# Performance work log

Measured on AMD Instinct MI355X. Metric: run time of the kernel, lower is better.

## Reference

```python
import jax, jax.numpy as jnp
import numpy as np

B, S, H, NH, HD = 2, 2048, 1024, 16, 64
THETA = 10000.0


def setup_inputs() -> dict:
    key = jax.random.key(0)
    k1, k2, k3, k4, k5 = jax.random.split(key, 5)
    hidden_states = jax.random.normal(k1, (B, S, H), dtype=jnp.float32)
    # RoPE tables, interleaved-pair layout: [c0,c0,c1,c1,...] along head_dim
    inv_freq = 1.0 / (THETA ** (jnp.arange(0, HD, 2, dtype=jnp.float32) / HD))
    t = jnp.arange(S, dtype=jnp.float32)
    freqs = jnp.outer(t, inv_freq)                      # [S, HD//2]
    freqs_cos = jnp.repeat(jnp.cos(freqs), 2, axis=-1)  # [S, HD]
    freqs_sin = jnp.repeat(jnp.sin(freqs), 2, axis=-1)  # [S, HD]
    position_ids = jnp.arange(S, dtype=jnp.int32)
    w = 0.02
    Wq = jax.random.normal(k2, (H, H), dtype=jnp.float32) * w
    Wk = jax.random.normal(k3, (H, H), dtype=jnp.float32) * w
    Wv = jax.random.normal(k4, (H, H), dtype=jnp.float32) * w
    Wo = jax.random.normal(k5, (H, H), dtype=jnp.float32) * w
    return {"hidden_states": hidden_states, "freqs_cos": freqs_cos,
            "freqs_sin": freqs_sin, "position_ids": position_ids,
            "Wq": Wq, "Wk": Wk, "Wv": Wv, "Wo": Wo}


def _rotate_half_interleaved(x):
    # stack([-x[..., 1::2], x[..., ::2]], -1).reshape_as(x)
    xe = x.reshape(x.shape[:-1] + (HD // 2, 2))
    return jnp.stack([-xe[..., 1], xe[..., 0]], axis=-1).reshape(x.shape)


def reference(hidden_states, freqs_cos, freqs_sin, position_ids, Wq, Wk, Wv, Wo):
    b, s, _ = hidden_states.shape
    # QKV projections (torch Linear: y = x @ W.T), split into heads [b, nh, s, hd]
    q = jnp.einsum('bsh,oh->bso', hidden_states, Wq).reshape(b, s, NH, HD).transpose(0, 2, 1, 3)
    k = jnp.einsum('bsh,oh->bso', hidden_states, Wk).reshape(b, s, NH, HD).transpose(0, 2, 1, 3)
    v = jnp.einsum('bsh,oh->bso', hidden_states, Wv).reshape(b, s, NH, HD).transpose(0, 2, 1, 3)
    cos = freqs_cos[position_ids][None, None]  # [1, 1, s, hd]
    sin = freqs_sin[position_ids][None, None]
    rq = _rotate_half_interleaved(q)
    # NOTE: faithful to source bug — rotate_half_k is built from q, not k
    q = q * cos + rq * sin
    k = k * cos + rq * sin
    # causal SDPA, scale = 1/sqrt(head_dim)
    scores = jnp.einsum('bhqd,bhkd->bhqk', q, k) / jnp.sqrt(jnp.float32(HD))
    causal = jnp.tril(jnp.ones((s, s), dtype=bool))
    scores = jnp.where(causal, scores, jnp.float32(-1e30))
    attn = jax.nn.softmax(scores, axis=-1)
    out = jnp.einsum('bhqk,bhkd->bhqd', attn, v)
    out = out.transpose(0, 2, 1, 3).reshape(b, s, H)
    return jnp.einsum('bsh,oh->bso', out, Wo)
```

## Files before the change

### kernel.cpp

```cpp
#include <hip/hip_runtime.h>
#include <stdint.h>

#define BB 2
#define SS 2048
#define HH 1024
#define NHH 16
#define HDD 64

typedef short bf16s;
typedef __attribute__((ext_vector_type(8))) short short8;
typedef __attribute__((ext_vector_type(4))) short short4v;
typedef __attribute__((ext_vector_type(2))) short short2v;
typedef __attribute__((ext_vector_type(4))) float f32x4;
typedef _Float16 half4v __attribute__((ext_vector_type(4)));
typedef _Float16 half8v __attribute__((ext_vector_type(8)));
typedef __fp16 fp16x2 __attribute__((ext_vector_type(2)));

__device__ inline short f2bf(float f) {
  union { float f; uint32_t u; } v; v.f = f;
  uint32_t r = (v.u + 0x7fffu + ((v.u >> 16) & 1u)) >> 16;
  return (short)r;
}
__device__ inline float bf2f(short h) {
  union { uint32_t u; float f; } v; v.u = ((uint32_t)(uint16_t)h) << 16;
  return v.f;
}

__device__ __forceinline__ float exp2_raw(float x) {
  float r;
  asm("v_exp_f32 %0, %1\n\ts_nop 0" : "=v"(r) : "v"(x));
  return r;
}

__device__ inline void gld_lds16(const void* g, void* l) {
  __builtin_amdgcn_global_load_lds((const __attribute__((address_space(1))) void*)g,
                                   (__attribute__((address_space(3))) void*)l, 16, 0, 0);
}

__device__ inline void stv(short* C, size_t i, float v) { C[i] = f2bf(v); }
__device__ inline void stv(float* C, size_t i, float v) { C[i] = v; }

__device__ inline f32x4 mfma_k32(short8 a, short8 b, f32x4 c) {
  return __builtin_amdgcn_mfma_f32_16x16x32_bf16(a, b, c, 0, 0, 0);
}
__device__ inline f32x4 mfma_k32(half8v a, half8v b, f32x4 c) {
  return __builtin_amdgcn_mfma_f32_16x16x32_f16(a, b, c, 0, 0, 0);
}
template <typename ET> struct ftr;
template <> struct ftr<short>     { using v8 = short8; };
template <> struct ftr<_Float16>  { using v8 = half8v; };

__global__ __launch_bounds__(256) void convert_all(
    const float* __restrict__ x, const float* __restrict__ Wq,
    const float* __restrict__ Wk, const float* __restrict__ Wv,
    const float* __restrict__ Wo, bf16s* __restrict__ xb,
    bf16s* __restrict__ wqkv, _Float16* __restrict__ wof) {
  const long M1 = 1024L * 1024L;
  long e = (long)(blockIdx.x * blockDim.x + threadIdx.x) * 4;
  if (e < 7 * M1) {
    const float* src; bf16s* dst;
    if (e < 4 * M1)      { src = x  + e;            dst = xb   + e; }
    else if (e < 5 * M1) { src = Wq + (e - 4 * M1); dst = wqkv + (e - 4 * M1); }
    else if (e < 6 * M1) { src = Wk + (e - 5 * M1); dst = wqkv + (e - 4 * M1); }
    else                 { src = Wv + (e - 6 * M1); dst = wqkv + (e - 4 * M1); }
    float4 v = *(const float4*)src;
    short4v o;
    o.x = f2bf(v.x); o.y = f2bf(v.y); o.z = f2bf(v.z); o.w = f2bf(v.w);
    *(short4v*)dst = o;
  } else {
    float4 v = *(const float4*)(Wo + (e - 7 * M1));
    half4v o;
    o.x = (_Float16)v.x; o.y = (_Float16)v.y;
    o.z = (_Float16)v.z; o.w = (_Float16)v.w;
    *(half4v*)(wof + (e - 7 * M1)) = o;
  }
}

template <typename ET, typename OT, int MT>
__global__ __launch_bounds__(256) void gemm_bt(
    const ET* __restrict__ A, const ET* __restrict__ Bm,
    OT* __restrict__ C, int K, int ldc) {
  using V8 = typename ftr<ET>::v8;
  __shared__ __align__(16) ET As[MT * 32 * 64];
  __shared__ __align__(16) ET Bs[128 * 64];
  const int tid = threadIdx.x;
  const int lane = tid & 63, w = tid >> 6;
  const int quad = lane >> 4, mcol = lane & 15;
  const int bm = blockIdx.y * (MT * 32), bn = blockIdx.x * 128;
  const int wm = (w >> 1) * (MT * 16), wn = (w & 1) * 64;
  f32x4 acc[MT][4] = {};
  const int nkt = K >> 6;
  for (int kt = 0; kt < nkt; ++kt) {
    __syncthreads();
#pragma unroll
    for (int i = 0; i < MT; ++i) {
      int seg = (i * 4 + w) * 512;
      int flat = seg + lane * 8;
      int row = flat >> 6;
      int cpos = (flat >> 3) & 7;
      int cs = cpos ^ (row & 7);
      gld_lds16(A + (size_t)(bm + row) * K + kt * 64 + cs * 8, &As[seg]);
    }
#pragma unroll
    for (int i = 0; i < 4; ++i) {
      int seg = (i * 4 + w) * 512;
      int flat = seg + lane * 8;
      int row = flat >> 6;
      int cpos = (flat >> 3) & 7;
      int cs = cpos ^ (row & 7);
      gld_lds16(Bm + (size_t)(bn + row) * K + kt * 64 + cs * 8, &Bs[seg]);
    }
    __syncthreads();
#pragma unroll
    for (int ks = 0; ks < 2; ++ks) {
      V8 af[MT], bf[4];
#pragma unroll
      for (int mt = 0; mt < MT; ++mt) {
        int row = wm + mt * 16 + mcol;
        int cs = (ks * 4 + quad) ^ (row & 7);
        af[mt] = *(const V8*)&As[row * 64 + cs * 8];
      }
#pragma unroll
      for (int nt = 0; nt < 4; ++nt) {
        int row = wn + nt * 16 + mcol;
        int cs = (ks * 4 + quad) ^ (row & 7);
        bf[nt] = *(const V8*)&Bs[row * 64 + cs * 8];
      }
#pragma unroll
      for (int mt = 0; mt < MT; ++mt)
#pragma unroll
        for (int nt = 0; nt < 4; ++nt)
          acc[mt][nt] = mfma_k32(af[mt], bf[nt], acc[mt][nt]);
    }
  }
#pragma unroll
  for (int mt = 0; mt < MT; ++mt)
#pragma unroll
    for (int nt = 0; nt < 4; ++nt) {
      int r0 = bm + wm + mt * 16 + quad * 4;
      int c = bn + wn + nt * 16 + mcol;
#pragma unroll
      for (int r = 0; r < 4; ++r)
        stv(C, (size_t)(r0 + r) * ldc + c, acc[mt][nt][r]);
    }
}

__global__ __launch_bounds__(256) void postproc(
    const bf16s* __restrict__ qkv, const float* __restrict__ fcos,
    const float* __restrict__ fsin, const int* __restrict__ pos,
    bf16s* __restrict__ Q, bf16s* __restrict__ Kc, _Float16* __restrict__ Vt) {
  const float LOG2E = 1.4426950408889634f;
  const int st = blockIdx.x, bh = blockIdx.y;
  const int b = bh >> 4, h = bh & 15;
  const int tid = threadIdx.x;
  const int m0 = b * 2048 + st * 64;
  {
    const int row = tid >> 2, pc = tid & 3;
    const int s = st * 64 + row;
    const int p = pos[s];
    const bf16s* qp = qkv + (size_t)(m0 + row) * 3072 + h * 64 + pc * 16;
    short8 qv[2] = { *(const short8*)qp, *(const short8*)(qp + 8) };
    short8 kv[2] = { *(const short8*)(qp + 1024), *(const short8*)(qp + 1032) };
    const float* cp = fcos + (size_t)p * 64 + pc * 16;
    const float* sp = fsin + (size_t)p * 64 + pc * 16;
    short8 qo[2], ko[2];
#pragma unroll
    for (int hf = 0; hf < 2; ++hf)
#pragma unroll
      for (int j = 0; j < 4; ++j) {
        float c = cp[hf * 8 + 2 * j], sn = sp[hf * 8 + 2 * j];
        float q0 = bf2f(qv[hf][2 * j]), q1 = bf2f(qv[hf][2 * j + 1]);
        float k0 = bf2f(kv[hf][2 * j]), k1 = bf2f(kv[hf][2 * j + 1]);
        qo[hf][2 * j]     = f2bf((q0 * c - q1 * sn) * 0.125f);
        qo[hf][2 * j + 1] = f2bf((q1 * c + q0 * sn) * 0.125f);
        ko[hf][2 * j]     = f2bf((k0 * c - q1 * sn) * LOG2E);
        ko[hf][2 * j + 1] = f2bf((k1 * c + q0 * sn) * LOG2E);
      }
    size_t o = ((size_t)bh * 2048 + s) * 64 + pc * 16;
    *(short8*)&Q[o] = qo[0];  *(short8*)&Q[o + 8] = qo[1];
    *(short8*)&Kc[o] = ko[0]; *(short8*)&Kc[o + 8] = ko[1];
  }
  __shared__ __align__(16) _Float16 T[64 * 72];
#pragma unroll
  for (int p2 = 0; p2 < 2; ++p2) {
    int sl = p2 * 32 + (tid >> 3);
    int ch = tid & 7;
    short8 v = *(const short8*)&qkv[(size_t)(m0 + sl) * 3072 + 2048 + h * 64 + ch * 8];
#pragma unroll
    for (int j = 0; j < 8; ++j) T[(ch * 8 + j) * 72 + sl] = (_Float16)bf2f(v[j]);
  }
  __syncthreads();
#pragma unroll
  for (int p2 = 0; p2 < 2; ++p2) {
    int dl = p2 * 32 + (tid >> 3);
    int ch = tid & 7;
    half8v v = *(const half8v*)&T[dl * 72 + ch * 8];
    *(half8v*)&Vt[((size_t)bh * 64 + dl) * 2048 + st * 64 + ch * 8] = v;
  }
}

template <bool DOB>
__device__ __forceinline__ void step2(
    const bf16s* __restrict__ Ks, const _Float16* __restrict__ Vp,
    const short8* bqA, const short8* bqB,
    f32x4* OA, f32x4* OB, float& lA, float& lB,
    bool diagA, bool diagB, int w, int quad, int col) {
  f32x4 sA[4], sB[4];
#pragma unroll
  for (int t = 0; t < 4; ++t) {
    f32x4 a = {}, bb = {};
#pragma unroll
    for (int ks = 0; ks < 2; ++ks) {
      int krow = t * 16 + col;
      int cs = (ks * 4 + quad) ^ (krow & 7);
      short8 af = *(const short8*)&Ks[krow * 64 + cs * 8];
      a = __builtin_amdgcn_mfma_f32_16x16x32_bf16(af, bqA[ks], a, 0, 0, 0);
      if (DOB) bb = __builtin_amdgcn_mfma_f32_16x16x32_bf16(af, bqB[ks], bb, 0, 0, 0);
    }
    sA[t] = a;
    if (DOB) sB[t] = bb;
  }
  if (diagA) {
#pragma unroll
    for (int t = 0; t < 4; ++t)
#pragma unroll
      for (int r = 0; r < 4; ++r)
        if (t * 16 + quad * 4 + r > w * 16 + col) sA[t][r] = -1e30f;
  }
  if (DOB && diagB) {
#pragma unroll
    for (int t = 0; t < 4; ++t)
#pragma unroll
      for (int r = 0; r < 4; ++r)
        if (t * 16 + quad * 4 + r > w * 16 + col) sB[t][r] = -1e30f;
  }
  half4v paA[4], paB[4];
#pragma unroll
  for (int t = 0; t < 4; ++t) {
    {
      float p0 = exp2_raw(sA[t][0]), p1 = exp2_raw(sA[t][1]);
      float p2 = exp2_raw(sA[t][2]), p3 = exp2_raw(sA[t][3]);
      lA += (p0 + p1) + (p2 + p3);
      union { fp16x2 h2[2]; half4v h4; } u;
      u.h2[0] = __builtin_amdgcn_cvt_pkrtz(p0, p1);
      u.h2[1] = __builtin_amdgcn_cvt_pkrtz(p2, p3);
      paA[t] = u.h4;
    }
    if (DOB) {
      float p0 = exp2_raw(sB[t][0]), p1 = exp2_raw(sB[t][1]);
      float p2 = exp2_raw(sB[t][2]), p3 = exp2_raw(sB[t][3]);
      lB += (p0 + p1) + (p2 + p3);
      union { fp16x2 h2[2]; half4v h4; } u;
      u.h2[0] = __builtin_amdgcn_cvt_pkrtz(p0, p1);
      u.h2[1] = __builtin_amdgcn_cvt_pkrtz(p2, p3);
      paB[t] = u.h4;
    }
  }
#pragma unroll
  for (int dt = 0; dt < 4; ++dt) {
    int vrow = dt * 16 + col;
    const _Float16* vp = &Vp[vrow * 72 + (quad ^ (vrow & 3)) * 16];
    union { half8v v8; half4v v4[2]; } a01, a23;
    a01.v8 = *(const half8v*)vp;
    a23.v8 = *(const half8v*)(vp + 8);
    half4v bv[4] = { a01.v4[0], a01.v4[1], a23.v4[0], a23.v4[1] };
#pragma unroll
    for (int t = 0; t < 4; ++t) {
      OA[dt] = __builtin_amdgcn_mfma_f32_16x16x16f16(paA[t], bv[t], OA[dt], 0, 0, 0);
      if (DOB) OB[dt] = __builtin_amdgcn_mfma_f32_16x16x16f16(paB[t], bv[t], OB[dt], 0, 0, 0);
    }
  }
}

__global__ __launch_bounds__(256) void attn(
    const bf16s* __restrict__ Q, const bf16s* __restrict__ Kb,
    const _Float16* __restrict__ Vt, _Float16* __restrict__ O) {
  __shared__ __align__(16) bf16s Ks[64 * 64];
  __shared__ __align__(16) _Float16 Vp[64 * 72];
  const int bh = blockIdx.y;
  const int tid = threadIdx.x, lane = tid & 63, w = tid >> 6;
  const int quad = lane >> 4, col = lane & 15;
  const size_t base = (size_t)bh * 2048 * 64;
  const _Float16* vbase = Vt + (size_t)bh * 64 * 2048;
  const int b = bh >> 4, h = bh & 15;
  const int x = blockIdx.x;
  const int qbA = 31 - x, qbB = x;

  short8 bqA[2], bqB[2];
  {
    const int qrA = qbA * 64 + w * 16 + col;
    const int qrB = qbB * 64 + w * 16 + col;
#pragma unroll
    for (int ks = 0; ks < 2; ++ks) {
      bqA[ks] = *(const short8*)&Q[base + (size_t)qrA * 64 + ks * 32 + quad * 8];
      bqB[ks] = *(const short8*)&Q[base + (size_t)qrB * 64 + ks * 32 + quad * 8];
    }
  }
  f32x4 OA[4] = {}, OB[4] = {};
  float lA = 0.f, lB = 0.f;

  const int vd = tid >> 2, vc = tid & 3;
  const int rot = vd & 3;
  for (int kt = 0; kt <= qbA; ++kt) {
    half8v vr0 = *(const half8v*)&vbase[(size_t)vd * 2048 + kt * 64 + vc * 16];
    half8v vr1 = *(const half8v*)&vbase[(size_t)vd * 2048 + kt * 64 + vc * 16 + 8];
    __syncthreads();
    {
      union { half8v v8; half4v v4[2]; } u0, u1;
      u0.v8 = vr0; u1.v8 = vr1;
      int rbase = vd * 72 + vc * 4;
      *(half4v*)&Vp[rbase + (0 ^ rot) * 16] = u0.v4[0];
      *(half4v*)&Vp[rbase + (1 ^ rot) * 16] = u0.v4[1];
      *(half4v*)&Vp[rbase + (2 ^ rot) * 16] = u1.v4[0];
      *(half4v*)&Vp[rbase + (3 ^ rot) * 16] = u1.v4[1];
    }
#pragma unroll
    for (int i = 0; i < 2; ++i) {
      int seg = (i * 4 + w) * 512;
      int flat = seg + lane * 8;
      int row = flat >> 6, cpos = (flat >> 3) & 7;
      int cs = cpos ^ (row & 7);
      gld_lds16(&Kb[base + (size_t)(kt * 64 + row) * 64 + cs * 8], &Ks[seg]);
    }
    __syncthreads();
    if (kt <= qbB)
      step2<true>(Ks, Vp, bqA, bqB, OA, OB, lA, lB,
                  false, kt == qbB, w, quad, col);
    else
      step2<false>(Ks, Vp, bqA, bqB, OA, OB, lA, lB,
                   kt == qbA, false, w, quad, col);
  }

  lA += __shfl_xor(lA, 16); lA += __shfl_xor(lA, 32);
  lB += __shfl_xor(lB, 16); lB += __shfl_xor(lB, 32);

#pragma unroll
  for (int which = 0; which < 2; ++which) {
    const int qb = which ? qbB : qbA;
    const f32x4* Oacc = which ? OB : OA;
    const float l = which ? lB : lA;
    float l4[4];
#pragma unroll
    for (int r = 0; r < 4; ++r) l4[r] = __shfl(l, quad * 4 + r);
#pragma unroll
    for (int dt = 0; dt < 4; ++dt)
#pragma unroll
      for (int r = 0; r < 4; ++r) {
        int srow = qb * 64 + w * 16 + quad * 4 + r;
        O[((size_t)b * 2048 + srow) * 1024 + h * 64 + dt * 16 + col] =
            (_Float16)(Oacc[dt][r] / l4[r]);
      }
  }
}

extern "C" void kernel_launch(void* const* d_in, const int* in_sizes, int n_in,
                              void* d_out, int out_size, void* d_ws, size_t ws_size,
                              hipStream_t stream) {
  (void)in_sizes; (void)n_in; (void)out_size; (void)ws_size;
  const float* x  = (const float*)d_in[0];
  const float* fc = (const float*)d_in[1];
  const float* fs = (const float*)d_in[2];
  const int* pos  = (const int*)d_in[3];
  const float* Wq = (const float*)d_in[4];
  const float* Wk = (const float*)d_in[5];
  const float* Wv = (const float*)d_in[6];
  const float* Wo = (const float*)d_in[7];
  float* out = (float*)d_out;
  char* ws = (char*)d_ws;
  const size_t MB = 1024 * 1024;
  bf16s* xb    = (bf16s*)(ws);
  bf16s* wqkv  = (bf16s*)(ws + 8 * MB);
  _Float16* wof = (_Float16*)(ws + 14 * MB);
  bf16s* qkv   = (bf16s*)(ws + 16 * MB);
  bf16s* Qb    = (bf16s*)(ws + 40 * MB);
  bf16s* Kb    = (bf16s*)(ws + 48 * MB);
  _Float16* Vt = (_Float16*)(ws + 56 * MB);
  _Float16* Ob = (_Float16*)(ws);

  convert_all<<<8192, 256, 0, stream>>>(x, Wq, Wk, Wv, Wo, xb, wqkv, wof);
  gemm_bt<short, short, 4><<<dim3(24, 32), 256, 0, stream>>>(xb, wqkv, qkv, 1024, 3072);
  postproc<<<dim3(32, 32), 256, 0, stream>>>(qkv, fc, fs, pos, Qb, Kb, Vt);
  attn<<<dim3(16, 32), 256, 0, stream>>>(Qb, Kb, Vt, Ob);
  gemm_bt<_Float16, float, 2><<<dim3(8, 64), 256, 0, stream>>>(Ob, wof, out, 1024, 1024);
}
```

Baseline: 191.3 us.

## Split paired query-block attention into one query block per workgroup

The attention kernel no longer pairs a short and a long causal query block in each workgroup. It now launches 32x32 workgroups that each handle a single query block, processed in reverse order so the heaviest blocks start first. The V tile layout in LDS also changes from a rotated 72-stride layout to a plain 68-stride layout with half4 loads. This drops the K-fragment sharing between the two query blocks and the workgroup-level load balancing, and relies on more workgroups and hardware scheduling to balance the causal work instead. The new LDS stride may also cause bank conflicts on the V reads.

Result: slower. 209.0 us (+9.3%).

```diff
diff --git a/kernel.cpp b/kernel.cpp
--- a/kernel.cpp
+++ b/kernel.cpp
@@ -199,121 +199,81 @@
   }
 }
 
-template <bool DOB>
-__device__ __forceinline__ void step2(
-    const bf16s* __restrict__ Ks, const _Float16* __restrict__ Vp,
-    const short8* bqA, const short8* bqB,
-    f32x4* OA, f32x4* OB, float& lA, float& lB,
-    bool diagA, bool diagB, int w, int quad, int col) {
-  f32x4 sA[4], sB[4];
+__device__ __forceinline__ void attn_step(
+    const bf16s* __restrict__ Ks, const _Float16* __restrict__ Vs,
+    const short8* bq, f32x4* Oacc, float& l, bool diag,
+    int w, int quad, int col) {
+  f32x4 sc[4];
 #pragma unroll
   for (int t = 0; t < 4; ++t) {
-    f32x4 a = {}, bb = {};
+    f32x4 s4 = {};
 #pragma unroll
     for (int ks = 0; ks < 2; ++ks) {
       int krow = t * 16 + col;
       int cs = (ks * 4 + quad) ^ (krow & 7);
       short8 af = *(const short8*)&Ks[krow * 64 + cs * 8];
-      a = __builtin_amdgcn_mfma_f32_16x16x32_bf16(af, bqA[ks], a, 0, 0, 0);
-      if (DOB) bb = __builtin_amdgcn_mfma_f32_16x16x32_bf16(af, bqB[ks], bb, 0, 0, 0);
-    }
-    sA[t] = a;
-    if (DOB) sB[t] = bb;
-  }
-  if (diagA) {
+      s4 = __builtin_amdgcn_mfma_f32_16x16x32_bf16(af, bq[ks], s4, 0, 0, 0);
+    }
+    sc[t] = s4;
+  }
+  if (diag) {
 #pragma unroll
     for (int t = 0; t < 4; ++t)
 #pragma unroll
       for (int r = 0; r < 4; ++r)
-        if (t * 16 + quad * 4 + r > w * 16 + col) sA[t][r] = -1e30f;
-  }
-  if (DOB && diagB) {
-#pragma unroll
-    for (int t = 0; t < 4; ++t)
-#pragma unroll
-      for (int r = 0; r < 4; ++r)
-        if (t * 16 + quad * 4 + r > w * 16 + col) sB[t][r] = -1e30f;
-  }
-  half4v paA[4], paB[4];
+        if (t * 16 + quad * 4 + r > w * 16 + col) sc[t][r] = -1e30f;
+  }
+  half4v pa[4];
 #pragma unroll
   for (int t = 0; t < 4; ++t) {
-    {
-      float p0 = exp2_raw(sA[t][0]), p1 = exp2_raw(sA[t][1]);
-      float p2 = exp2_raw(sA[t][2]), p3 = exp2_raw(sA[t][3]);
-      lA += (p0 + p1) + (p2 + p3);
-      union { fp16x2 h2[2]; half4v h4; } u;
-      u.h2[0] = __builtin_amdgcn_cvt_pkrtz(p0, p1);
-      u.h2[1] = __builtin_amdgcn_cvt_pkrtz(p2, p3);
-      paA[t] = u.h4;
-    }
-    if (DOB) {
-      float p0 = exp2_raw(sB[t][0]), p1 = exp2_raw(sB[t][1]);
-      float p2 = exp2_raw(sB[t][2]), p3 = exp2_raw(sB[t][3]);
-      lB += (p0 + p1) + (p2 + p3);
-      union { fp16x2 h2[2]; half4v h4; } u;
-      u.h2[0] = __builtin_amdgcn_cvt_pkrtz(p0, p1);
-      u.h2[1] = __builtin_amdgcn_cvt_pkrtz(p2, p3);
-      paB[t] = u.h4;
-    }
-  }
-#pragma unroll
-  for (int dt = 0; dt < 4; ++dt) {
-    int vrow = dt * 16 + col;
-    const _Float16* vp = &Vp[vrow * 72 + (quad ^ (vrow & 3)) * 16];
-    union { half8v v8; half4v v4[2]; } a01, a23;
-    a01.v8 = *(const half8v*)vp;
-    a23.v8 = *(const half8v*)(vp + 8);
-    half4v bv[4] = { a01.v4[0], a01.v4[1], a23.v4[0], a23.v4[1] };
-#pragma unroll
-    for (int t = 0; t < 4; ++t) {
-      OA[dt] = __builtin_amdgcn_mfma_f32_16x16x16f16(paA[t], bv[t], OA[dt], 0, 0, 0);
-      if (DOB) OB[dt] = __builtin_amdgcn_mfma_f32_16x16x16f16(paB[t], bv[t], OB[dt], 0, 0, 0);
-    }
-  }
+    float p0 = exp2_raw(sc[t][0]), p1 = exp2_raw(sc[t][1]);
+    float p2 = exp2_raw(sc[t][2]), p3 = exp2_raw(sc[t][3]);
+    l += (p0 + p1) + (p2 + p3);
+    union { fp16x2 h2[2]; half4v h4; } u;
+    u.h2[0] = __builtin_amdgcn_cvt_pkrtz(p0, p1);
+    u.h2[1] = __builtin_amdgcn_cvt_pkrtz(p2, p3);
+    pa[t] = u.h4;
+  }
+#pragma unroll
+  for (int t = 0; t < 4; ++t)
+#pragma unroll
+    for (int dt = 0; dt < 4; ++dt) {
+      int vrow = dt * 16 + col;
+      half4v bv = *(const half4v*)&Vs[vrow * 68 + t * 16 + quad * 4];
+      Oacc[dt] = __builtin_amdgcn_mfma_f32_16x16x16f16(pa[t], bv, Oacc[dt], 0, 0, 0);
+    }
 }
 
 __global__ __launch_bounds__(256) void attn(
     const bf16s* __restrict__ Q, const bf16s* __restrict__ Kb,
     const _Float16* __restrict__ Vt, _Float16* __restrict__ O) {
   __shared__ __align__(16) bf16s Ks[64 * 64];
-  __shared__ __align__(16) _Float16 Vp[64 * 72];
+  __shared__ __align__(16) _Float16 Vs[64 * 68];
   const int bh = blockIdx.y;
   const int tid = threadIdx.x, lane = tid & 63, w = tid >> 6;
   const int quad = lane >> 4, col = lane & 15;
   const size_t base = (size_t)bh * 2048 * 64;
   const _Float16* vbase = Vt + (size_t)bh * 64 * 2048;
   const int b = bh >> 4, h = bh & 15;
-  const int x = blockIdx.x;
-  const int qbA = 31 - x, qbB = x;
-
-  short8 bqA[2], bqB[2];
+  const int qb = 31 - (int)blockIdx.x;
+
+  short8 bq[2];
   {
-    const int qrA = qbA * 64 + w * 16 + col;
-    const int qrB = qbB * 64 + w * 16 + col;
-#pragma unroll
-    for (int ks = 0; ks < 2; ++ks) {
-      bqA[ks] = *(const short8*)&Q[base + (size_t)qrA * 64 + ks * 32 + quad * 8];
-      bqB[ks] = *(const short8*)&Q[base + (size_t)qrB * 64 + ks * 32 + quad * 8];
-    }
-  }
-  f32x4 OA[4] = {}, OB[4] = {};
-  float lA = 0.f, lB = 0.f;
+    const int qrow = qb * 64 + w * 16 + col;
+#pragma unroll
+    for (int ks = 0; ks < 2; ++ks)
+      bq[ks] = *(const short8*)&Q[base + (size_t)qrow * 64 + ks * 32 + quad * 8];
+  }
+  f32x4 Oacc[4] = {};
+  float l = 0.f;
 
   const int vd = tid >> 2, vc = tid & 3;
-  const int rot = vd & 3;
-  for (int kt = 0; kt <= qbA; ++kt) {
+  for (int kt = 0; kt <= qb; ++kt) {
     half8v vr0 = *(const half8v*)&vbase[(size_t)vd * 2048 + kt * 64 + vc * 16];
     half8v vr1 = *(const half8v*)&vbase[(size_t)vd * 2048 + kt * 64 + vc * 16 + 8];
     __syncthreads();
-    {
-      union { half8v v8; half4v v4[2]; } u0, u1;
-      u0.v8 = vr0; u1.v8 = vr1;
-      int rbase = vd * 72 + vc * 4;
-      *(half4v*)&Vp[rbase + (0 ^ rot) * 16] = u0.v4[0];
-      *(half4v*)&Vp[rbase + (1 ^ rot) * 16] = u0.v4[1];
-      *(half4v*)&Vp[rbase + (2 ^ rot) * 16] = u1.v4[0];
-      *(half4v*)&Vp[rbase + (3 ^ rot) * 16] = u1.v4[1];
-    }
+    *(half8v*)&Vs[vd * 68 + vc * 16] = vr0;
+    *(half8v*)&Vs[vd * 68 + vc * 16 + 8] = vr1;
 #pragma unroll
     for (int i = 0; i < 2; ++i) {
       int seg = (i * 4 + w) * 512;
@@ -323,34 +283,21 @@
       gld_lds16(&Kb[base + (size_t)(kt * 64 + row) * 64 + cs * 8], &Ks[seg]);
     }
     __syncthreads();
-    if (kt <= qbB)
-      step2<true>(Ks, Vp, bqA, bqB, OA, OB, lA, lB,
-                  false, kt == qbB, w, quad, col);
-    else
-      step2<false>(Ks, Vp, bqA, bqB, OA, OB, lA, lB,
-                   kt == qbA, false, w, quad, col);
-  }
-
-  lA += __shfl_xor(lA, 16); lA += __shfl_xor(lA, 32);
-  lB += __shfl_xor(lB, 16); lB += __shfl_xor(lB, 32);
-
-#pragma unroll
-  for (int which = 0; which < 2; ++which) {
-    const int qb = which ? qbB : qbA;
-    const f32x4* Oacc = which ? OB : OA;
-    const float l = which ? lB : lA;
-    float l4[4];
-#pragma unroll
-    for (int r = 0; r < 4; ++r) l4[r] = __shfl(l, quad * 4 + r);
-#pragma unroll
-    for (int dt = 0; dt < 4; ++dt)
-#pragma unroll
-      for (int r = 0; r < 4; ++r) {
-        int srow = qb * 64 + w * 16 + quad * 4 + r;
-        O[((size_t)b * 2048 + srow) * 1024 + h * 64 + dt * 16 + col] =
-            (_Float16)(Oacc[dt][r] / l4[r]);
-      }
-  }
+    attn_step(Ks, Vs, bq, Oacc, l, kt == qb, w, quad, col);
+  }
+
+  l += __shfl_xor(l, 16); l += __shfl_xor(l, 32);
+  float l4[4];
+#pragma unroll
+  for (int r = 0; r < 4; ++r) l4[r] = __shfl(l, quad * 4 + r);
+#pragma unroll
+  for (int dt = 0; dt < 4; ++dt)
+#pragma unroll
+    for (int r = 0; r < 4; ++r) {
+      int srow = qb * 64 + w * 16 + quad * 4 + r;
+      O[((size_t)b * 2048 + srow) * 1024 + h * 64 + dt * 16 + col] =
+          (_Float16)(Oacc[dt][r] / l4[r]);
+    }
 }
 
 extern "C" void kernel_launch(void* const* d_in, const int* in_sizes, int n_in,
@@ -380,6 +327,6 @@
   convert_all<<<8192, 256, 0, stream>>>(x, Wq, Wk, Wv, Wo, xb, wqkv, wof);
   gemm_bt<short, short, 4><<<dim3(24, 32), 256, 0, stream>>>(xb, wqkv, qkv, 1024, 3072);
   postproc<<<dim3(32, 32), 256, 0, stream>>>(qkv, fc, fs, pos, Qb, Kb, Vt);
-  attn<<<dim3(16, 32), 256, 0, stream>>>(Qb, Kb, Vt, Ob);
+  attn<<<dim3(32, 32), 256, 0, stream>>>(Qb, Kb, Vt, Ob);
   gemm_bt<_Float16, float, 2><<<dim3(8, 64), 256, 0, stream>>>(Ob, wof, out, 1024, 1024);
 }
```

## Double-buffer K/V tiles in LDS and prefetch next tile during compute

Applied to the files above, without the earlier changes.

Keeps two LDS buffers for the K and V tiles. While the current tile is being computed, the next K tile is loaded asynchronously into the other buffer, and the next V tile is loaded into registers and written to LDS after compute. This removes one barrier per iteration and hides global-load latency behind the MFMA work. The V LDS layout also changes from a swizzled 72-stride to a padded 68-stride with direct half4 reads. The costs are double the LDS footprint, which may reduce occupancy, plus more live registers, and the new V reads may hit bank conflicts.

After: 196.4 us. 1.03x slower.

```diff
diff --git a/kernel.cpp b/kernel.cpp
--- a/kernel.cpp
+++ b/kernel.cpp
@@ -201,7 +201,7 @@
 
 template <bool DOB>
 __device__ __forceinline__ void step2(
-    const bf16s* __restrict__ Ks, const _Float16* __restrict__ Vp,
+    const bf16s* __restrict__ Ks, const _Float16* __restrict__ Vs,
     const short8* bqA, const short8* bqB,
     f32x4* OA, f32x4* OB, float& lA, float& lB,
     bool diagA, bool diagB, int w, int quad, int col) {
@@ -257,26 +257,21 @@
     }
   }
 #pragma unroll
-  for (int dt = 0; dt < 4; ++dt) {
-    int vrow = dt * 16 + col;
-    const _Float16* vp = &Vp[vrow * 72 + (quad ^ (vrow & 3)) * 16];
-    union { half8v v8; half4v v4[2]; } a01, a23;
-    a01.v8 = *(const half8v*)vp;
-    a23.v8 = *(const half8v*)(vp + 8);
-    half4v bv[4] = { a01.v4[0], a01.v4[1], a23.v4[0], a23.v4[1] };
-#pragma unroll
-    for (int t = 0; t < 4; ++t) {
-      OA[dt] = __builtin_amdgcn_mfma_f32_16x16x16f16(paA[t], bv[t], OA[dt], 0, 0, 0);
-      if (DOB) OB[dt] = __builtin_amdgcn_mfma_f32_16x16x16f16(paB[t], bv[t], OB[dt], 0, 0, 0);
-    }
-  }
+  for (int t = 0; t < 4; ++t)
+#pragma unroll
+    for (int dt = 0; dt < 4; ++dt) {
+      int vrow = dt * 16 + col;
+      half4v bv = *(const half4v*)&Vs[vrow * 68 + t * 16 + quad * 4];
+      OA[dt] = __builtin_amdgcn_mfma_f32_16x16x16f16(paA[t], bv, OA[dt], 0, 0, 0);
+      if (DOB) OB[dt] = __builtin_amdgcn_mfma_f32_16x16x16f16(paB[t], bv, OB[dt], 0, 0, 0);
+    }
 }
 
 __global__ __launch_bounds__(256) void attn(
     const bf16s* __restrict__ Q, const bf16s* __restrict__ Kb,
     const _Float16* __restrict__ Vt, _Float16* __restrict__ O) {
-  __shared__ __align__(16) bf16s Ks[64 * 64];
-  __shared__ __align__(16) _Float16 Vp[64 * 72];
+  __shared__ __align__(16) bf16s Ks[2][64 * 64];
+  __shared__ __align__(16) _Float16 Vs[2][64 * 68];
   const int bh = blockIdx.y;
   const int tid = threadIdx.x, lane = tid & 63, w = tid >> 6;
   const int quad = lane >> 4, col = lane & 15;
@@ -300,35 +295,52 @@
   float lA = 0.f, lB = 0.f;
 
   const int vd = tid >> 2, vc = tid & 3;
-  const int rot = vd & 3;
-  for (int kt = 0; kt <= qbA; ++kt) {
-    half8v vr0 = *(const half8v*)&vbase[(size_t)vd * 2048 + kt * 64 + vc * 16];
-    half8v vr1 = *(const half8v*)&vbase[(size_t)vd * 2048 + kt * 64 + vc * 16 + 8];
-    __syncthreads();
-    {
-      union { half8v v8; half4v v4[2]; } u0, u1;
-      u0.v8 = vr0; u1.v8 = vr1;
-      int rbase = vd * 72 + vc * 4;
-      *(half4v*)&Vp[rbase + (0 ^ rot) * 16] = u0.v4[0];
-      *(half4v*)&Vp[rbase + (1 ^ rot) * 16] = u0.v4[1];
-      *(half4v*)&Vp[rbase + (2 ^ rot) * 16] = u1.v4[0];
-      *(half4v*)&Vp[rbase + (3 ^ rot) * 16] = u1.v4[1];
-    }
+  const _Float16* vsrc = vbase + (size_t)vd * 2048 + vc * 16;
+  const int voff = vd * 68 + vc * 16;
+
+  {
+    half8v a0 = *(const half8v*)(vsrc);
+    half8v a1 = *(const half8v*)(vsrc + 8);
+    *(half8v*)&Vs[0][voff] = a0;
+    *(half8v*)&Vs[0][voff + 8] = a1;
 #pragma unroll
     for (int i = 0; i < 2; ++i) {
       int seg = (i * 4 + w) * 512;
       int flat = seg + lane * 8;
       int row = flat >> 6, cpos = (flat >> 3) & 7;
       int cs = cpos ^ (row & 7);
-      gld_lds16(&Kb[base + (size_t)(kt * 64 + row) * 64 + cs * 8], &Ks[seg]);
-    }
+      gld_lds16(&Kb[base + (size_t)row * 64 + cs * 8], &Ks[0][seg]);
+    }
+  }
+
+  for (int kt = 0; kt <= qbA; ++kt) {
+    const int cur = kt & 1;
     __syncthreads();
+    half8v n0, n1;
+    const bool pf = (kt < qbA);
+    if (pf) {
+      n0 = *(const half8v*)(vsrc + (size_t)(kt + 1) * 64);
+      n1 = *(const half8v*)(vsrc + (size_t)(kt + 1) * 64 + 8);
+#pragma unroll
+      for (int i = 0; i < 2; ++i) {
+        int seg = (i * 4 + w) * 512;
+        int flat = seg + lane * 8;
+        int row = flat >> 6, cpos = (flat >> 3) & 7;
+        int cs = cpos ^ (row & 7);
+        gld_lds16(&Kb[base + (size_t)((kt + 1) * 64 + row) * 64 + cs * 8],
+                  &Ks[cur ^ 1][seg]);
+      }
+    }
     if (kt <= qbB)
-      step2<true>(Ks, Vp, bqA, bqB, OA, OB, lA, lB,
+      step2<true>(Ks[cur], Vs[cur], bqA, bqB, OA, OB, lA, lB,
                   false, kt == qbB, w, quad, col);
     else
-      step2<false>(Ks, Vp, bqA, bqB, OA, OB, lA, lB,
+      step2<false>(Ks[cur], Vs[cur], bqA, bqB, OA, OB, lA, lB,
                    kt == qbA, false, w, quad, col);
+    if (pf) {
+      *(half8v*)&Vs[cur ^ 1][voff] = n0;
+      *(half8v*)&Vs[cur ^ 1][voff + 8] = n1;
+    }
   }
 
   lA += __shfl_xor(lA, 16); lA += __shfl_xor(lA, 32);
```
